# Performance work log

Measured on AMD Instinct MI355X. Metric: run time of the kernel, lower is better.

The kernel has to match this reference:

```python
import jax, jax.numpy as jnp
import numpy as np

B, TE, TD, EH, DH = 128, 512, 128, 512, 512
K_CNN, C_CNN = 7, 105

def setup_inputs() -> dict:
    key = jax.random.key(0)
    ks = jax.random.split(key, 20)
    n = lambda k, shp: jax.random.normal(k, shp, dtype=jnp.float32) * 0.05
    return {
        "LSTM": jax.random.normal(ks[0], (B, TE, EH), dtype=jnp.float32),
        "CNNs": jax.random.normal(ks[1], (B, K_CNN, C_CNN), dtype=jnp.float32),
        "Wa_w": n(ks[2], (TD, DH)), "Wa_b": n(ks[3], (TD,)),
        "Ua_w": n(ks[4], (TE, EH)), "Ua_b": n(ks[5], (TE,)),
        "va_w": n(ks[6], (1, TE + TD)), "va_b": n(ks[7], (1,)),
        "phi_w": n(ks[8], (EH, TE)), "phi_b": n(ks[9], (EH,)),
        "Wih": n(ks[10], (4 * DH, C_CNN + EH)), "Whh": n(ks[11], (4 * DH, DH)),
        "bih": n(ks[12], (4 * DH,)), "bhh": n(ks[13], (4 * DH,)),
        "wij_w": n(ks[14], (K_CNN, DH + C_CNN)), "wij_b": n(ks[15], (K_CNN,)),
        "s_i": jax.random.uniform(ks[16], (B, DH), dtype=jnp.float32),
        "m_i": jax.random.uniform(ks[17], (B, DH), dtype=jnp.float32),
    }

def reference(LSTM, CNNs, Wa_w, Wa_b, Ua_w, Ua_b, va_w, va_b, phi_w, phi_b,
              Wih, Whh, bih, bhh, wij_w, wij_b, s_i, m_i):
    Bn, Te, Eh = LSTM.shape
    Td = Wa_w.shape[0]
    Dh = s_i.shape[1]
    # delta_i_j for all j: strict lower-triangular one-hots [Te, Te]
    Dm = jnp.tril(jnp.ones((Te, Te), LSTM.dtype), k=-1)
    phi = Dm @ phi_w.T + phi_b                     # [Te, Eh]
    ph = phi[None, :, :] * LSTM                    # [B, Te, Eh] phi_delta * LSTM[:, j]
    Ua = jnp.einsum('bte,se->bts', ph, Ua_w) + Ua_b  # [B, Te, Te]
    Wa = s_i @ Wa_w.T + Wa_b                       # [B, Td] (same for all i, j)
    cat = jnp.concatenate([jnp.broadcast_to(Wa[:, None, :], (Bn, Te, Td)), Ua], axis=-1)
    Cw = jnp.tanh(cat) * va_w[0]                   # [B, Te, Td+Te]
    # one-hot mask picks index i + Te - j; v_a reduces to a single gathered term + bias
    idx = jnp.arange(Td)[:, None] + Te - jnp.arange(Te)[None, :]   # [Td, Te]
    e = Cw[:, jnp.arange(Te)[None, :], idx] + va_b[0]              # [B, Td, Te]
    a = jax.nn.softmax(e, axis=-1)
    c_i = jnp.einsum('bit,bte->bie', a, LSTM)      # [B, Td, Eh]
    # CNN attention (same for all decoder steps; note non-standard normalizer kept faithfully)
    w_cnn, w_s = wij_w[:, :C_CNN], wij_w[:, C_CNN:]
    ep = jnp.tanh(jnp.einsum('bkc,kc->bk', CNNs, w_cnn) + s_i @ w_s.T + wij_b)  # [B, K]
    ap = jnp.exp(ep) / jnp.sum(ep)
    c_p = jnp.einsum('bk,bkc->bc', ap, CNNs)       # [B, C_CNN]
    # LSTMCell with fixed (s_i, m_i) state => all decoder steps vectorize over i
    x = jnp.concatenate([c_i, jnp.broadcast_to(c_p[:, None, :], (Bn, Td, C_CNN))], axis=-1)
    gates = jnp.einsum('bid,gd->big', x, Wih) + bih + (s_i @ Whh.T + bhh)[:, None, :]
    ig, fg, gg, og = jnp.split(gates, 4, axis=-1)
    cnew = jax.nn.sigmoid(fg) * m_i[:, None, :] + jax.nn.sigmoid(ig) * jnp.tanh(gg)
    h = jax.nn.sigmoid(og) * jnp.tanh(cnew)        # [B, Td, Dh]
    return h
```

## Files before the change

### kernel.cpp

```cpp
#include <hip/hip_runtime.h>
#include <hip/hip_bf16.h>

#define B_   128
#define TE_  512
#define TD_  128
#define EH_  512
#define DH_  512
#define KC_  7
#define CC_  105
#define G_   2048
#define KX_  617
#define KP_  640

typedef __attribute__((ext_vector_type(8))) short bf16x8;
typedef __attribute__((ext_vector_type(4))) float f32x4;

__device__ __forceinline__ float sigm(float x){ return 1.f/(1.f + __expf(-x)); }
__device__ __forceinline__ float tanhf_fast(float x){
  float e = __expf(2.f*x);
  return 1.f - 2.f/(e + 1.f);
}

__device__ __forceinline__ unsigned short f2bf(float f){
  unsigned int u = __float_as_uint(f);
  unsigned int r = (u + 0x7fffu + ((u >> 16) & 1u)) >> 16;
  return (unsigned short)r;
}

__device__ __forceinline__ float dot512f(const float* a, const float* b) {
  const float4* a4 = (const float4*)a; const float4* b4 = (const float4*)b;
  float acc = 0.f;
  #pragma unroll 8
  for (int q = 0; q < 128; ++q) {
    float4 x = a4[q], y = b4[q];
    acc += x.x*y.x + x.y*y.y + x.z*y.z + x.w*y.w;
  }
  return acc;
}

static const size_t OFF_PHI  = 0;
static const size_t OFF_WA   = OFF_PHI  + (size_t)TE_*EH_*4;
static const size_t OFF_HPRE = OFF_WA   + (size_t)B_*TD_*4;
static const size_t OFF_EP   = OFF_HPRE + (size_t)B_*G_*4;
static const size_t OFF_CP   = OFF_EP   + 4096;
static const size_t OFF_ET   = ((OFF_CP + (size_t)B_*CC_*4 + 255)/256)*256;
static const size_t OFF_STAT = OFF_ET + (size_t)B_*TE_*TD_*4;
static const size_t OFF_P    = ((OFF_STAT + (size_t)2*B_*TD_*4 + 255)/256)*256;
static const size_t OFF_LT   = OFF_P  + (size_t)B_*TD_*TE_*2;
static const size_t OFF_WR   = OFF_LT + (size_t)B_*TE_*EH_*2;
static const size_t OFF_PT   = OFF_P;
static const size_t OFF_SUM  = OFF_PT + (size_t)TE_*EH_*4;

__global__ __launch_bounds__(256) void k_trw(const float* __restrict__ phi_w,
                                             float* __restrict__ phiT) {
  int e0 = blockIdx.x * 64, t0 = blockIdx.y * 64;
  __shared__ float tile[64][65];
  int tid = threadIdx.x;
  int r = tid >> 2, c16 = (tid & 3) * 16;
  const float4* src = (const float4*)(phi_w + (size_t)(e0 + r)*TE_ + t0 + c16);
  float4 v0 = src[0], v1 = src[1], v2 = src[2], v3 = src[3];
  *(float4*)&tile[r][c16]    = v0;
  *(float4*)&tile[r][c16+4]  = v1;
  *(float4*)&tile[r][c16+8]  = v2;
  *(float4*)&tile[r][c16+12] = v3;
  __syncthreads();
  float o[16];
  #pragma unroll
  for (int j = 0; j < 16; ++j) o[j] = tile[c16+j][r];
  float* dst = phiT + (size_t)(t0 + r)*EH_ + e0 + c16;
  *(float4*)dst      = *(float4*)&o[0];
  *(float4*)(dst+4)  = *(float4*)&o[4];
  *(float4*)(dst+8)  = *(float4*)&o[8];
  *(float4*)(dst+12) = *(float4*)&o[12];
}

__global__ void k_phiA(const float* __restrict__ phiT, float* __restrict__ phi,
                       float* __restrict__ sums) {
  int e = blockIdx.x * 256 + threadIdx.x;
  int z = blockIdx.y;
  float acc = 0.f;
  for (int t = z*64; t < z*64 + 64; ++t) {
    phi[(size_t)t*EH_ + e] = acc;
    acc += phiT[(size_t)t*EH_ + e];
  }
  sums[z*EH_ + e] = acc;
}
__global__ void k_phiB(const float* __restrict__ sums, const float* __restrict__ phi_b,
                       float* __restrict__ phi) {
  int e = blockIdx.x * 256 + threadIdx.x;
  int z = blockIdx.y;
  float off = phi_b[e];
  for (int zz = 0; zz < z; ++zz) off += sums[zz*EH_ + e];
  for (int t = z*64; t < z*64 + 64; ++t)
    phi[(size_t)t*EH_ + e] += off;
}

__global__ void k_wa(const float* __restrict__ s_i, const float* __restrict__ Wa_w,
                     const float* __restrict__ Wa_b, const float* __restrict__ va_w,
                     float* __restrict__ wa) {
  int id = blockIdx.x * blockDim.x + threadIdx.x;
  int b = id >> 7, d = id & 127;
  float acc = Wa_b[d] + dot512f(s_i + (size_t)b*DH_, Wa_w + (size_t)d*DH_);
  wa[id] = tanhf_fast(acc) * va_w[d];
}

__global__ void k_hpre(const float* __restrict__ s_i, const float* __restrict__ Whh,
                       const float* __restrict__ bih, const float* __restrict__ bhh,
                       float* __restrict__ hpre) {
  int id = blockIdx.x * blockDim.x + threadIdx.x;
  int b = id >> 11, g = id & 2047;
  hpre[id] = bih[g] + bhh[g] + dot512f(s_i + (size_t)b*DH_, Whh + (size_t)g*DH_);
}

__global__ __launch_bounds__(256) void k_ep(const float* __restrict__ CNNs,
                                            const float* __restrict__ wij_w,
                                            const float* __restrict__ wij_b,
                                            const float* __restrict__ s_i,
                                            float* __restrict__ ep) {
  int gw = blockIdx.x * 4 + (threadIdx.x >> 6);
  int lane = threadIdx.x & 63;
  if (gw >= B_*KC_) return;
  int b = gw / KC_, k = gw % KC_;
  const float* cr = CNNs + (size_t)(b*KC_ + k)*CC_;
  const float* wr = wij_w + (size_t)k*KX_;
  float acc = 0.f;
  for (int c = lane; c < CC_; c += 64) acc += cr[c] * wr[c];
  const float* sr = s_i + (size_t)b*DH_;
  const float* wsr = wr + CC_;
  #pragma unroll
  for (int j = 0; j < 8; ++j) { int h = lane + j*64; acc += sr[h] * wsr[h]; }
  #pragma unroll
  for (int m = 32; m; m >>= 1) acc += __shfl_xor(acc, m, 64);
  if (lane == 0) ep[gw] = tanhf_fast(acc + wij_b[k]);
}

__global__ void k_cnn_fin(const float* __restrict__ ep, const float* __restrict__ CNNs,
                          float* __restrict__ cp) {
  __shared__ float red[1024];
  __shared__ float apl[B_*KC_];
  int tid = threadIdx.x;
  red[tid] = (tid < B_*KC_) ? ep[tid] : 0.f;
  __syncthreads();
  for (int off = 512; off > 0; off >>= 1) {
    if (tid < off) red[tid] += red[tid + off];
    __syncthreads();
  }
  float S = red[0];
  if (tid < B_*KC_) apl[tid] = __expf(ep[tid]) / S;
  __syncthreads();
  for (int idx = tid; idx < B_*CC_; idx += blockDim.x) {
    int b = idx / CC_, c = idx % CC_;
    float acc = 0.f;
    #pragma unroll
    for (int k = 0; k < KC_; ++k)
      acc += apl[b*KC_ + k] * CNNs[(size_t)(b*KC_ + k)*CC_ + c];
    cp[idx] = acc;
  }
}

__global__ void k_cvtW(const float* __restrict__ Wih, unsigned short* __restrict__ Wr) {
  int id = blockIdx.x * 256 + threadIdx.x;
  int nr = id / 80, c8 = (id % 80) * 8;
  int gate = nr & 3, dh = nr >> 2;
  const float* src = Wih + (size_t)(gate*DH_ + dh)*KX_;
  unsigned short o[8];
  #pragma unroll
  for (int j = 0; j < 8; ++j) {
    int col = c8 + j;
    o[j] = (col < KX_) ? f2bf(src[col]) : 0;
  }
  *(uint4*)(Wr + (size_t)nr*KP_ + c8) = *(uint4*)o;
}

__global__ __launch_bounds__(256) void k_ltrans(const float* __restrict__ LSTM,
                                                unsigned short* __restrict__ LT) {
  int e0 = blockIdx.x * 64, t0 = blockIdx.y * 64, b = blockIdx.z;
  __shared__ float tile[64][65];
  int tid = threadIdx.x;
  int tt = tid >> 2, c16 = (tid & 3) * 16;
  const float4* src = (const float4*)(LSTM + ((size_t)b*TE_ + t0 + tt)*EH_ + e0 + c16);
  float4 v0 = src[0], v1 = src[1], v2 = src[2], v3 = src[3];
  *(float4*)&tile[tt][c16]    = v0;
  *(float4*)&tile[tt][c16+4]  = v1;
  *(float4*)&tile[tt][c16+8]  = v2;
  *(float4*)&tile[tt][c16+12] = v3;
  __syncthreads();
  int e = tid >> 2, t16 = (tid & 3) * 16;
  unsigned short o[16];
  #pragma unroll
  for (int j = 0; j < 16; ++j) o[j] = f2bf(tile[t16+j][e]);
  unsigned short* dst = LT + ((size_t)b*EH_ + e0 + e)*TE_ + t0 + t16;
  *(uint4*)dst     = *(uint4*)&o[0];
  *(uint4*)(dst+8) = *(uint4*)&o[8];
}

#define BMM_M 64
#define LDA_  40
#define LDB_  40
__global__ __launch_bounds__(256) void k_bandmm(const float* __restrict__ LSTM,
                                                const float* __restrict__ phi,
                                                const float* __restrict__ Ua_w,
                                                const float* __restrict__ Ua_b,
                                                const float* __restrict__ va_w,
                                                const float* __restrict__ va_b,
                                                const float* __restrict__ wa,
                                                float* __restrict__ ET) {
  int t0 = blockIdx.x * BMM_M;
  int b  = blockIdx.y;
  int s_base = 321 - t0;
  __shared__ short sA[BMM_M * LDA_];
  __shared__ short sB[192 * LDB_];
  int tid = threadIdx.x;
  int wave = tid >> 6, lane = tid & 63;
  int quad = lane >> 4, l16 = lane & 15;

  f32x4 acc[4][3];
  #pragma unroll
  for (int m = 0; m < 4; ++m)
    #pragma unroll
    for (int n = 0; n < 3; ++n)
      acc[m][n] = (f32x4){0.f, 0.f, 0.f, 0.f};

  int arow = tid >> 2;
  int ach  = (tid & 3) * 8;
  int aq   = ach >> 2;

  const float4* baseL = (const float4*)(LSTM + ((size_t)b*TE_ + t0 + arow)*EH_);
  const float4* baseP = (const float4*)(phi + (size_t)(t0 + arow)*EH_);
  const float4* baseU[3];
  int brow[3], bch[3];
  #pragma unroll
  for (int c = 0; c < 3; ++c) {
    int idx = c*256 + tid;
    brow[c] = idx >> 2;
    bch[c]  = (idx & 3) * 8;
    int s = s_base + brow[c];
    int sc = s < 0 ? 0 : (s > 511 ? 511 : s);
    baseU[c] = (const float4*)(Ua_w + (size_t)sc*EH_ + bch[c]);
  }

  float4 l0 = baseL[aq], l1 = baseL[aq+1], p0 = baseP[aq], p1 = baseP[aq+1];
  float4 u0[3], u1[3];
  #pragma unroll
  for (int c = 0; c < 3; ++c) { u0[c] = baseU[c][0]; u1[c] = baseU[c][1]; }

  for (int k0 = 0; k0 < EH_; k0 += 32) {
    unsigned short at[8];
    at[0]=f2bf(l0.x*p0.x); at[1]=f2bf(l0.y*p0.y); at[2]=f2bf(l0.z*p0.z); at[3]=f2bf(l0.w*p0.w);
    at[4]=f2bf(l1.x*p1.x); at[5]=f2bf(l1.y*p1.y); at[6]=f2bf(l1.z*p1.z); at[7]=f2bf(l1.w*p1.w);
    unsigned short bt[3][8];
    #pragma unroll
    for (int c = 0; c < 3; ++c) {
      bt[c][0]=f2bf(u0[c].x); bt[c][1]=f2bf(u0[c].y); bt[c][2]=f2bf(u0[c].z); bt[c][3]=f2bf(u0[c].w);
      bt[c][4]=f2bf(u1[c].x); bt[c][5]=f2bf(u1[c].y); bt[c][6]=f2bf(u1[c].z); bt[c][7]=f2bf(u1[c].w);
    }
    if (k0 + 32 < EH_) {
      int q = (k0 + 32) >> 2;
      l0 = baseL[q+aq]; l1 = baseL[q+aq+1]; p0 = baseP[q+aq]; p1 = baseP[q+aq+1];
      #pragma unroll
      for (int c = 0; c < 3; ++c) { u0[c] = baseU[c][q]; u1[c] = baseU[c][q+1]; }
    }
    __syncthreads();
    *(uint4*)&sA[arow*LDA_ + ach] = *(uint4*)at;
    #pragma unroll
    for (int c = 0; c < 3; ++c)
      *(uint4*)&sB[brow[c]*LDB_ + bch[c]] = *(uint4*)bt[c];
    __syncthreads();
    bf16x8 bfr[3];
    #pragma unroll
    for (int n = 0; n < 3; ++n)
      bfr[n] = *(const bf16x8*)&sB[(l16 + (wave*3 + n)*16)*LDB_ + quad*8];
    #pragma unroll
    for (int m = 0; m < 4; ++m) {
      bf16x8 af = *(const bf16x8*)&sA[(l16 + m*16)*LDA_ + quad*8];
      #pragma unroll
      for (int n = 0; n < 3; ++n)
        acc[m][n] = __builtin_amdgcn_mfma_f32_16x16x32_bf16(af, bfr[n], acc[m][n], 0, 0, 0);
    }
  }

  float vb = va_b[0];
  #pragma unroll
  for (int n = 0; n < 3; ++n) {
    int s = s_base + wave*48 + n*16 + l16;
    float ub = (s >= 0 && s < TE_) ? Ua_b[s] : 0.f;
    float vw = (s >= 0 && s < TE_) ? va_w[TD_ + s] : 0.f;
    #pragma unroll
    for (int m = 0; m < 4; ++m) {
      #pragma unroll
      for (int r = 0; r < 4; ++r) {
        int t = t0 + m*16 + quad*4 + r;
        int i = s + t - 384;
        if (i >= 0 && i < TD_) {
          float val;
          if (s >= 0) val = tanhf_fast(acc[m][n][r] + ub) * vw + vb;
          else        val = wa[b*TD_ + s + 128] + vb;
          ET[((size_t)b*TE_ + t)*TD_ + i] = val;
        }
      }
    }
  }
}

__global__ __launch_bounds__(256) void k_stats(const float* __restrict__ ET,
                                               float* __restrict__ stat) {
  int i0 = blockIdx.x * 64, b = blockIdx.y;
  __shared__ float red[4][64], smax[64];
  int tid = threadIdx.x;
  int q = tid >> 6, il = tid & 63;
  const float* col = ET + (size_t)b*TE_*TD_ + i0 + il;
  float m = -1e30f;
  for (int t = q*128; t < q*128 + 128; ++t) m = fmaxf(m, col[(size_t)t*TD_]);
  red[q][il] = m;
  __syncthreads();
  if (tid < 64) {
    float mm = fmaxf(fmaxf(red[0][tid], red[1][tid]), fmaxf(red[2][tid], red[3][tid]));
    smax[tid] = mm;
  }
  __syncthreads();
  float mm = smax[il];
  float s = 0.f;
  for (int t = q*128; t < q*128 + 128; ++t) s += __expf(col[(size_t)t*TD_] - mm);
  __syncthreads();
  red[q][il] = s;
  __syncthreads();
  if (tid < 64) {
    float ss = red[0][tid] + red[1][tid] + red[2][tid] + red[3][tid];
    stat[b*TD_ + i0 + tid] = smax[tid];
    stat[(size_t)B_*TD_ + b*TD_ + i0 + tid] = 1.f/ss;
  }
}

__global__ __launch_bounds__(256) void k_trP(const float* __restrict__ ET,
                                             const float* __restrict__ stat,
                                             unsigned short* __restrict__ P) {
  int t0 = blockIdx.x * 64, i0 = blockIdx.y * 64, b = blockIdx.z;
  __shared__ float tile[64][65];
  __shared__ float smL[64], svL[64];
  int tid = threadIdx.x;
  if (tid < 64) {
    smL[tid] = stat[b*TD_ + i0 + tid];
    svL[tid] = stat[(size_t)B_*TD_ + b*TD_ + i0 + tid];
  }
  int tt = tid >> 2, c16 = (tid & 3) * 16;
  const float4* src = (const float4*)(ET + ((size_t)b*TE_ + t0 + tt)*TD_ + i0 + c16);
  float4 v[4]; v[0] = src[0]; v[1] = src[1]; v[2] = src[2]; v[3] = src[3];
  __syncthreads();
  const float* vf = (const float*)v;
  #pragma unroll
  for (int j = 0; j < 16; ++j)
    tile[tt][c16+j] = __expf(vf[j] - smL[c16+j]) * svL[c16+j];
  __syncthreads();
  int i = tid >> 2, t16 = (tid & 3) * 16;
  unsigned short o[16];
  #pragma unroll
  for (int j = 0; j < 16; ++j) o[j] = f2bf(tile[t16+j][i]);
  unsigned short* dst = P + ((size_t)b*TD_ + i0 + i)*TE_ + t0 + t16;
  *(uint4*)dst     = *(uint4*)&o[0];
  *(uint4*)(dst+8) = *(uint4*)&o[8];
}

__global__ void k_cp_fill(const float* __restrict__ cp, unsigned short* __restrict__ X) {
  int id = blockIdx.x * 256 + threadIdx.x;
  int m = id >> 4, c8 = (id & 15) * 8;
  int b = m >> 7;
  unsigned short o[8];
  #pragma unroll
  for (int j = 0; j < 8; ++j) {
    int c = c8 + j;
    o[j] = (c < CC_) ? f2bf(cp[b*CC_ + c]) : 0;
  }
  *(uint4*)(X + (size_t)m*KP_ + EH_ + c8) = *(uint4*)o;
}

#define CI_LD 40
__global__ __launch_bounds__(256) void k_ci_mm(const unsigned short* __restrict__ P,
                                               const unsigned short* __restrict__ LT,
                                               unsigned short* __restrict__ X) {
  int b = blockIdx.x, e0 = blockIdx.y * 128;
  __shared__ short sA[128 * CI_LD];
  __shared__ short sB[128 * CI_LD];
  int tid = threadIdx.x;
  int wave = tid >> 6, lane = tid & 63, quad = lane >> 4, l16 = lane & 15;
  int wm = wave >> 1, wn = wave & 1;
  int row = tid >> 1, ho = (tid & 1) * 16;

  const unsigned short* pa = P + ((size_t)b*TD_ + row)*TE_ + ho;
  const unsigned short* pb = LT + ((size_t)b*EH_ + e0 + row)*TE_ + ho;

  f32x4 acc[4][4];
  #pragma unroll
  for (int m = 0; m < 4; ++m)
    #pragma unroll
    for (int n = 0; n < 4; ++n)
      acc[m][n] = (f32x4){0.f, 0.f, 0.f, 0.f};

  uint4 a0 = *(const uint4*)pa, a1 = *(const uint4*)(pa + 8);
  uint4 b0 = *(const uint4*)pb, b1 = *(const uint4*)(pb + 8);

  for (int k0 = 0; k0 < TE_; k0 += 32) {
    uint4 na0, na1, nb0, nb1;
    if (k0 + 32 < TE_) {
      na0 = *(const uint4*)(pa + k0 + 32); na1 = *(const uint4*)(pa + k0 + 40);
      nb0 = *(const uint4*)(pb + k0 + 32); nb1 = *(const uint4*)(pb + k0 + 40);
    }
    __syncthreads();
    *(uint4*)&sA[row*CI_LD + ho]     = a0;
    *(uint4*)&sA[row*CI_LD + ho + 8] = a1;
    *(uint4*)&sB[row*CI_LD + ho]     = b0;
    *(uint4*)&sB[row*CI_LD + ho + 8] = b1;
    __syncthreads();
    bf16x8 bfr[4];
    #pragma unroll
    for (int n = 0; n < 4; ++n)
      bfr[n] = *(const bf16x8*)&sB[(wn*64 + n*16 + l16)*CI_LD + quad*8];
    #pragma unroll
    for (int m = 0; m < 4; ++m) {
      bf16x8 af = *(const bf16x8*)&sA[(wm*64 + m*16 + l16)*CI_LD + quad*8];
      #pragma unroll
      for (int n = 0; n < 4; ++n)
        acc[m][n] = __builtin_amdgcn_mfma_f32_16x16x32_bf16(af, bfr[n], acc[m][n], 0, 0, 0);
    }
    a0 = na0; a1 = na1; b0 = nb0; b1 = nb1;
  }

  #pragma unroll
  for (int m = 0; m < 4; ++m) {
    int i = wm*64 + m*16 + quad*4;
    #pragma unroll
    for (int n = 0; n < 4; ++n) {
      int e = e0 + wn*64 + n*16 + l16;
      unsigned short* xp = X + ((size_t)b*TD_ + i)*KP_ + e;
      #pragma unroll
      for (int r = 0; r < 4; ++r)
        xp[(size_t)r*KP_] = f2bf(acc[m][n][r]);
    }
  }
}

__global__ __launch_bounds__(256) void k_gates_mm(const unsigned short* __restrict__ Wr,
                                                  const unsigned short* __restrict__ X,
                                                  const float* __restrict__ hpre,
                                                  const float* __restrict__ m_i,
                                                  float* __restrict__ out) {
  int g0 = blockIdx.x * 128;
  int mi0 = blockIdx.y * 128;
  __shared__ short sA[128 * CI_LD];
  __shared__ short sB[128 * CI_LD];
  int tid = threadIdx.x;
  int wave = tid >> 6, lane = tid & 63, quad = lane >> 4, l16 = lane & 15;
  int wg = wave >> 1, wmi = wave & 1;
  int row = tid >> 1, ho = (tid & 1) * 16;

  const unsigned short* pa = Wr + (size_t)(g0 + row)*KP_ + ho;
  const unsigned short* pb = X + (size_t)(mi0 + row)*KP_ + ho;

  f32x4 acc[4][4];
  #pragma unroll
  for (int m = 0; m < 4; ++m)
    #pragma unroll
    for (int n = 0; n < 4; ++n)
      acc[m][n] = (f32x4){0.f, 0.f, 0.f, 0.f};

  uint4 a0 = *(const uint4*)pa, a1 = *(const uint4*)(pa + 8);
  uint4 b0 = *(const uint4*)pb, b1 = *(const uint4*)(pb + 8);

  for (int k0 = 0; k0 < KP_; k0 += 32) {
    uint4 na0, na1, nb0, nb1;
    if (k0 + 32 < KP_) {
      na0 = *(const uint4*)(pa + k0 + 32); na1 = *(const uint4*)(pa + k0 + 40);
      nb0 = *(const uint4*)(pb + k0 + 32); nb1 = *(const uint4*)(pb + k0 + 40);
    }
    __syncthreads();
    *(uint4*)&sA[row*CI_LD + ho]     = a0;
    *(uint4*)&sA[row*CI_LD + ho + 8] = a1;
    *(uint4*)&sB[row*CI_LD + ho]     = b0;
    *(uint4*)&sB[row*CI_LD + ho + 8] = b1;
    __syncthreads();
    bf16x8 bfr[4];
    #pragma unroll
    for (int n = 0; n < 4; ++n)
      bfr[n] = *(const bf16x8*)&sB[(wmi*64 + n*16 + l16)*CI_LD + quad*8];
    #pragma unroll
    for (int m = 0; m < 4; ++m) {
      bf16x8 af = *(const bf16x8*)&sA[(wg*64 + m*16 + l16)*CI_LD + quad*8];
      #pragma unroll
      for (int n = 0; n < 4; ++n)
        acc[m][n] = __builtin_amdgcn_mfma_f32_16x16x32_bf16(af, bfr[n], acc[m][n], 0, 0, 0);
    }
    a0 = na0; a1 = na1; b0 = nb0; b1 = nb1;
  }

  int bbk = mi0 >> 7;
  const float* hp = hpre + (size_t)bbk*G_;
  #pragma unroll
  for (int m = 0; m < 4; ++m) {
    int dh = (g0 >> 2) + wg*16 + m*4 + quad;
    float h0 = hp[dh], h1 = hp[DH_ + dh], h2 = hp[2*DH_ + dh], h3 = hp[3*DH_ + dh];
    float miv = m_i[(size_t)bbk*DH_ + dh];
    #pragma unroll
    for (int n = 0; n < 4; ++n) {
      int mi = mi0 + wmi*64 + n*16 + l16;
      float ig = acc[m][n][0] + h0;
      float fg = acc[m][n][1] + h1;
      float gg = acc[m][n][2] + h2;
      float og = acc[m][n][3] + h3;
      float c  = sigm(fg)*miv + sigm(ig)*tanhf_fast(gg);
      float h  = sigm(og)*tanhf_fast(c);
      out[(size_t)mi*DH_ + dh] = h;
    }
  }
}

extern "C" void kernel_launch(void* const* d_in, const int* in_sizes, int n_in,
                              void* d_out, int out_size, void* d_ws, size_t ws_size,
                              hipStream_t stream) {
  (void)in_sizes; (void)n_in; (void)out_size; (void)ws_size;
  const float* LSTM  = (const float*)d_in[0];
  const float* CNNs  = (const float*)d_in[1];
  const float* Wa_w  = (const float*)d_in[2];
  const float* Wa_b  = (const float*)d_in[3];
  const float* Ua_w  = (const float*)d_in[4];
  const float* Ua_b  = (const float*)d_in[5];
  const float* va_w  = (const float*)d_in[6];
  const float* va_b  = (const float*)d_in[7];
  const float* phi_w = (const float*)d_in[8];
  const float* phi_b = (const float*)d_in[9];
  const float* Wih   = (const float*)d_in[10];
  const float* Whh   = (const float*)d_in[11];
  const float* bih   = (const float*)d_in[12];
  const float* bhh   = (const float*)d_in[13];
  const float* wij_w = (const float*)d_in[14];
  const float* wij_b = (const float*)d_in[15];
  const float* s_i   = (const float*)d_in[16];
  const float* m_i   = (const float*)d_in[17];
  float* out = (float*)d_out;
  char* ws = (char*)d_ws;

  float* phi  = (float*)(ws + OFF_PHI);
  float* wa   = (float*)(ws + OFF_WA);
  float* hpre = (float*)(ws + OFF_HPRE);
  float* ep   = (float*)(ws + OFF_EP);
  float* cp   = (float*)(ws + OFF_CP);
  float* stat = (float*)(ws + OFF_STAT);
  float* ET   = (float*)(ws + OFF_ET);
  unsigned short* X  = (unsigned short*)(ws + OFF_ET);
  unsigned short* P  = (unsigned short*)(ws + OFF_P);
  unsigned short* LT = (unsigned short*)(ws + OFF_LT);
  unsigned short* Wr = (unsigned short*)(ws + OFF_WR);
  float* phiT        = (float*)(ws + OFF_PT);
  float* sums        = (float*)(ws + OFF_SUM);

  k_trw     <<<dim3(8,8),      dim3(256),  0, stream>>>(phi_w, phiT);
  k_phiA    <<<dim3(2,8),      dim3(256),  0, stream>>>(phiT, phi, sums);
  k_phiB    <<<dim3(2,8),      dim3(256),  0, stream>>>(sums, phi_b, phi);
  k_wa      <<<dim3(64),       dim3(256),  0, stream>>>(s_i, Wa_w, Wa_b, va_w, wa);
  k_hpre    <<<dim3(1024),     dim3(256),  0, stream>>>(s_i, Whh, bih, bhh, hpre);
  k_ep      <<<dim3(224),      dim3(256),  0, stream>>>(CNNs, wij_w, wij_b, s_i, ep);
  k_cnn_fin <<<dim3(1),        dim3(1024), 0, stream>>>(ep, CNNs, cp);
  k_cvtW    <<<dim3(640),      dim3(256),  0, stream>>>(Wih, Wr);
  k_ltrans  <<<dim3(8,8,128),  dim3(256),  0, stream>>>(LSTM, LT);
  k_bandmm  <<<dim3(8,128),    dim3(256),  0, stream>>>(LSTM, phi, Ua_w, Ua_b, va_w, va_b, wa, ET);
  k_stats   <<<dim3(2,128),    dim3(256),  0, stream>>>(ET, stat);
  k_trP     <<<dim3(8,2,128),  dim3(256),  0, stream>>>(ET, stat, P);
  k_cp_fill <<<dim3(1024),     dim3(256),  0, stream>>>(cp, X);
  k_ci_mm   <<<dim3(128,4),    dim3(256),  0, stream>>>(P, LT, X);
  k_gates_mm<<<dim3(16,128),   dim3(256),  0, stream>>>(Wr, X, hpre, m_i, out);
}
```

Before: 575.9 us.

## Rewrite gates GEMM with 256x256 tiles, direct-to-LDS loads, pre-convert Ua to bf16

The gates GEMM is replaced with a 512-thread kernel using 256x256 output tiles, K-tiles of 64, double-buffered LDS filled via global_load_lds with an XOR swizzle, and setprio around the MFMA bursts. The larger tile is meant to improve data reuse, and the async LDS loads cut register staging. Separately, Ua_w is converted to bf16 once in a new small kernel, so the band matmul loads half the bytes and skips per-iteration conversion. The trade-offs are much higher LDS use per block (128KB), more registers, and fewer blocks (512) to spread across the CUs.

```diff
diff --git a/kernel.cpp b/kernel.cpp
--- a/kernel.cpp
+++ b/kernel.cpp
@@ -11,6 +11,7 @@
 #define G_   2048
 #define KX_  617
 #define KP_  640
+#define GNT  10
 
 typedef __attribute__((ext_vector_type(8))) short bf16x8;
 typedef __attribute__((ext_vector_type(4))) float f32x4;
@@ -36,6 +37,12 @@
     acc += x.x*y.x + x.y*y.y + x.z*y.z + x.w*y.w;
   }
   return acc;
+}
+
+typedef __attribute__((address_space(3))) unsigned int lds_u32_t;
+typedef __attribute__((address_space(1))) const unsigned int glb_u32_t;
+__device__ __forceinline__ void gload16(const void* g, void* l) {
+  __builtin_amdgcn_global_load_lds((glb_u32_t*)g, (lds_u32_t*)l, 16, 0, 0);
 }
 
 static const size_t OFF_PHI  = 0;
@@ -50,6 +57,7 @@
 static const size_t OFF_WR   = OFF_LT + (size_t)B_*TE_*EH_*2;
 static const size_t OFF_PT   = OFF_P;
 static const size_t OFF_SUM  = OFF_PT + (size_t)TE_*EH_*4;
+static const size_t OFF_UB   = OFF_P + (size_t)1536*1024;
 
 __global__ __launch_bounds__(256) void k_trw(const float* __restrict__ phi_w,
                                              float* __restrict__ phiT) {
@@ -172,6 +180,15 @@
   *(uint4*)(Wr + (size_t)nr*KP_ + c8) = *(uint4*)o;
 }
 
+__global__ void k_cvtU(const float* __restrict__ Ua_w, unsigned short* __restrict__ Ub) {
+  int id = blockIdx.x * 256 + threadIdx.x;
+  const float4* s = (const float4*)Ua_w + (size_t)id*2;
+  float4 a = s[0], b = s[1];
+  unsigned short o[8] = {f2bf(a.x),f2bf(a.y),f2bf(a.z),f2bf(a.w),
+                         f2bf(b.x),f2bf(b.y),f2bf(b.z),f2bf(b.w)};
+  *(uint4*)(Ub + (size_t)id*8) = *(uint4*)o;
+}
+
 __global__ __launch_bounds__(256) void k_ltrans(const float* __restrict__ LSTM,
                                                 unsigned short* __restrict__ LT) {
   int e0 = blockIdx.x * 64, t0 = blockIdx.y * 64, b = blockIdx.z;
@@ -199,7 +216,7 @@
 #define LDB_  40
 __global__ __launch_bounds__(256) void k_bandmm(const float* __restrict__ LSTM,
                                                 const float* __restrict__ phi,
-                                                const float* __restrict__ Ua_w,
+                                                const unsigned short* __restrict__ Ub,
                                                 const float* __restrict__ Ua_b,
                                                 const float* __restrict__ va_w,
                                                 const float* __restrict__ va_b,
@@ -227,7 +244,7 @@
 
   const float4* baseL = (const float4*)(LSTM + ((size_t)b*TE_ + t0 + arow)*EH_);
   const float4* baseP = (const float4*)(phi + (size_t)(t0 + arow)*EH_);
-  const float4* baseU[3];
+  const unsigned short* ubase[3];
   int brow[3], bch[3];
   #pragma unroll
   for (int c = 0; c < 3; ++c) {
@@ -236,35 +253,32 @@
     bch[c]  = (idx & 3) * 8;
     int s = s_base + brow[c];
     int sc = s < 0 ? 0 : (s > 511 ? 511 : s);
-    baseU[c] = (const float4*)(Ua_w + (size_t)sc*EH_ + bch[c]);
+    ubase[c] = Ub + (size_t)sc*EH_ + bch[c];
   }
 
   float4 l0 = baseL[aq], l1 = baseL[aq+1], p0 = baseP[aq], p1 = baseP[aq+1];
-  float4 u0[3], u1[3];
-  #pragma unroll
-  for (int c = 0; c < 3; ++c) { u0[c] = baseU[c][0]; u1[c] = baseU[c][1]; }
+  uint4 ub0[3];
+  #pragma unroll
+  for (int c = 0; c < 3; ++c) ub0[c] = *(const uint4*)(ubase[c]);
 
   for (int k0 = 0; k0 < EH_; k0 += 32) {
     unsigned short at[8];
     at[0]=f2bf(l0.x*p0.x); at[1]=f2bf(l0.y*p0.y); at[2]=f2bf(l0.z*p0.z); at[3]=f2bf(l0.w*p0.w);
     at[4]=f2bf(l1.x*p1.x); at[5]=f2bf(l1.y*p1.y); at[6]=f2bf(l1.z*p1.z); at[7]=f2bf(l1.w*p1.w);
-    unsigned short bt[3][8];
-    #pragma unroll
-    for (int c = 0; c < 3; ++c) {
-      bt[c][0]=f2bf(u0[c].x); bt[c][1]=f2bf(u0[c].y); bt[c][2]=f2bf(u0[c].z); bt[c][3]=f2bf(u0[c].w);
-      bt[c][4]=f2bf(u1[c].x); bt[c][5]=f2bf(u1[c].y); bt[c][6]=f2bf(u1[c].z); bt[c][7]=f2bf(u1[c].w);
-    }
+    uint4 ust[3];
+    #pragma unroll
+    for (int c = 0; c < 3; ++c) ust[c] = ub0[c];
     if (k0 + 32 < EH_) {
       int q = (k0 + 32) >> 2;
       l0 = baseL[q+aq]; l1 = baseL[q+aq+1]; p0 = baseP[q+aq]; p1 = baseP[q+aq+1];
       #pragma unroll
-      for (int c = 0; c < 3; ++c) { u0[c] = baseU[c][q]; u1[c] = baseU[c][q+1]; }
+      for (int c = 0; c < 3; ++c) ub0[c] = *(const uint4*)(ubase[c] + k0 + 32);
     }
     __syncthreads();
     *(uint4*)&sA[arow*LDA_ + ach] = *(uint4*)at;
     #pragma unroll
     for (int c = 0; c < 3; ++c)
-      *(uint4*)&sB[brow[c]*LDB_ + bch[c]] = *(uint4*)bt[c];
+      *(uint4*)&sB[brow[c]*LDB_ + bch[c]] = ust[c];
     __syncthreads();
     bf16x8 bfr[3];
     #pragma unroll
@@ -438,73 +452,94 @@
   }
 }
 
-__global__ __launch_bounds__(256) void k_gates_mm(const unsigned short* __restrict__ Wr,
-                                                  const unsigned short* __restrict__ X,
-                                                  const float* __restrict__ hpre,
-                                                  const float* __restrict__ m_i,
-                                                  float* __restrict__ out) {
-  int g0 = blockIdx.x * 128;
-  int mi0 = blockIdx.y * 128;
-  __shared__ short sA[128 * CI_LD];
-  __shared__ short sB[128 * CI_LD];
-  int tid = threadIdx.x;
-  int wave = tid >> 6, lane = tid & 63, quad = lane >> 4, l16 = lane & 15;
-  int wg = wave >> 1, wmi = wave & 1;
-  int row = tid >> 1, ho = (tid & 1) * 16;
-
-  const unsigned short* pa = Wr + (size_t)(g0 + row)*KP_ + ho;
-  const unsigned short* pb = X + (size_t)(mi0 + row)*KP_ + ho;
-
-  f32x4 acc[4][4];
-  #pragma unroll
-  for (int m = 0; m < 4; ++m)
-    #pragma unroll
-    for (int n = 0; n < 4; ++n)
-      acc[m][n] = (f32x4){0.f, 0.f, 0.f, 0.f};
-
-  uint4 a0 = *(const uint4*)pa, a1 = *(const uint4*)(pa + 8);
-  uint4 b0 = *(const uint4*)pb, b1 = *(const uint4*)(pb + 8);
-
-  for (int k0 = 0; k0 < KP_; k0 += 32) {
-    uint4 na0, na1, nb0, nb1;
-    if (k0 + 32 < KP_) {
-      na0 = *(const uint4*)(pa + k0 + 32); na1 = *(const uint4*)(pa + k0 + 40);
-      nb0 = *(const uint4*)(pb + k0 + 32); nb1 = *(const uint4*)(pb + k0 + 40);
-    }
-    __syncthreads();
-    *(uint4*)&sA[row*CI_LD + ho]     = a0;
-    *(uint4*)&sA[row*CI_LD + ho + 8] = a1;
-    *(uint4*)&sB[row*CI_LD + ho]     = b0;
-    *(uint4*)&sB[row*CI_LD + ho + 8] = b1;
-    __syncthreads();
-    bf16x8 bfr[4];
-    #pragma unroll
-    for (int n = 0; n < 4; ++n)
-      bfr[n] = *(const bf16x8*)&sB[(wmi*64 + n*16 + l16)*CI_LD + quad*8];
-    #pragma unroll
-    for (int m = 0; m < 4; ++m) {
-      bf16x8 af = *(const bf16x8*)&sA[(wg*64 + m*16 + l16)*CI_LD + quad*8];
+__global__ __launch_bounds__(512, 2) void k_gates8(const unsigned short* __restrict__ Wr,
+                                                   const unsigned short* __restrict__ X,
+                                                   const float* __restrict__ hpre,
+                                                   const float* __restrict__ m_i,
+                                                   float* __restrict__ out) {
+  __shared__ short lds[4 * 256 * 64];
+  const int g0  = blockIdx.x * 256;
+  const int mi0 = blockIdx.y * 256;
+  const int tid  = threadIdx.x;
+  const int wave = tid >> 6, lane = tid & 63;
+  const int l16 = lane & 15, quad = lane >> 4;
+  const int wr = wave >> 2, wc = wave & 3;
+
+  const int srow8 = lane >> 3;
+  const int sch   = (lane & 7) ^ srow8;
+  const unsigned short* gA = Wr + (size_t)(g0  + wave*8 + srow8) * KP_ + sch*8;
+  const unsigned short* gB = X  + (size_t)(mi0 + wave*8 + srow8) * KP_ + sch*8;
+  short* lA0 = lds;
+  short* lB0 = lds + 16384;
+  short* lA1 = lds + 32768;
+  short* lB1 = lds + 49152;
+
+  f32x4 acc[8][4];
+  #pragma unroll
+  for (int m = 0; m < 8; ++m)
+    #pragma unroll
+    for (int n = 0; n < 4; ++n) acc[m][n] = (f32x4){0.f, 0.f, 0.f, 0.f};
+
+  auto stage = [&](int kt, int bf) {
+    short* la = bf ? lA1 : lA0;
+    short* lb = bf ? lB1 : lB0;
+    const unsigned short* ga = gA + kt*64;
+    const unsigned short* gb = gB + kt*64;
+    #pragma unroll
+    for (int r = 0; r < 4; ++r) {
+      gload16(ga + (size_t)r*64*KP_, la + (r*8 + wave)*512);
+      gload16(gb + (size_t)r*64*KP_, lb + (r*8 + wave)*512);
+    }
+  };
+
+  stage(0, 0);
+  __syncthreads();
+
+  const int x7 = l16 & 7;
+  for (int kt = 0; kt < GNT; ++kt) {
+    const int cur = kt & 1;
+    if (kt + 1 < GNT) stage(kt + 1, cur ^ 1);
+    const short* la = cur ? lA1 : lA0;
+    const short* lb = cur ? lB1 : lB0;
+    #pragma unroll
+    for (int ks = 0; ks < 2; ++ks) {
+      const int ck = ((((ks << 2) | quad) ^ x7) << 3);
+      bf16x8 bv[4];
       #pragma unroll
       for (int n = 0; n < 4; ++n)
-        acc[m][n] = __builtin_amdgcn_mfma_f32_16x16x32_bf16(af, bfr[n], acc[m][n], 0, 0, 0);
-    }
-    a0 = na0; a1 = na1; b0 = nb0; b1 = nb1;
-  }
-
-  int bbk = mi0 >> 7;
-  const float* hp = hpre + (size_t)bbk*G_;
-  #pragma unroll
-  for (int m = 0; m < 4; ++m) {
-    int dh = (g0 >> 2) + wg*16 + m*4 + quad;
+        bv[n] = *(const bf16x8*)&lb[(wc*64 + n*16 + l16)*64 + ck];
+      #pragma unroll
+      for (int qm = 0; qm < 2; ++qm) {
+        bf16x8 av[4];
+        #pragma unroll
+        for (int m = 0; m < 4; ++m)
+          av[m] = *(const bf16x8*)&la[(wr*128 + qm*64 + m*16 + l16)*64 + ck];
+        __builtin_amdgcn_s_setprio(1);
+        #pragma unroll
+        for (int m = 0; m < 4; ++m)
+          #pragma unroll
+          for (int n = 0; n < 4; ++n)
+            acc[qm*4 + m][n] = __builtin_amdgcn_mfma_f32_16x16x32_bf16(av[m], bv[n], acc[qm*4 + m][n], 0, 0, 0);
+        __builtin_amdgcn_s_setprio(0);
+      }
+    }
+    __syncthreads();
+  }
+
+  const int bb = (mi0 >> 7) + (wc >> 1);
+  const float* hp = hpre + (size_t)bb * G_;
+  #pragma unroll
+  for (int M = 0; M < 8; ++M) {
+    const int dh = (g0 >> 2) + wr*32 + M*4 + quad;
     float h0 = hp[dh], h1 = hp[DH_ + dh], h2 = hp[2*DH_ + dh], h3 = hp[3*DH_ + dh];
-    float miv = m_i[(size_t)bbk*DH_ + dh];
+    float miv = m_i[(size_t)bb*DH_ + dh];
     #pragma unroll
     for (int n = 0; n < 4; ++n) {
-      int mi = mi0 + wmi*64 + n*16 + l16;
-      float ig = acc[m][n][0] + h0;
-      float fg = acc[m][n][1] + h1;
-      float gg = acc[m][n][2] + h2;
-      float og = acc[m][n][3] + h3;
+      int mi = mi0 + wc*64 + n*16 + l16;
+      float ig = acc[M][n][0] + h0;
+      float fg = acc[M][n][1] + h1;
+      float gg = acc[M][n][2] + h2;
+      float og = acc[M][n][3] + h3;
       float c  = sigm(fg)*miv + sigm(ig)*tanhf_fast(gg);
       float h  = sigm(og)*tanhf_fast(c);
       out[(size_t)mi*DH_ + dh] = h;
@@ -550,6 +585,7 @@
   unsigned short* Wr = (unsigned short*)(ws + OFF_WR);
   float* phiT        = (float*)(ws + OFF_PT);
   float* sums        = (float*)(ws + OFF_SUM);
+  unsigned short* Ub = (unsigned short*)(ws + OFF_UB);
 
   k_trw     <<<dim3(8,8),      dim3(256),  0, stream>>>(phi_w, phiT);
   k_phiA    <<<dim3(2,8),      dim3(256),  0, stream>>>(phiT, phi, sums);
@@ -559,11 +595,12 @@
   k_ep      <<<dim3(224),      dim3(256),  0, stream>>>(CNNs, wij_w, wij_b, s_i, ep);
   k_cnn_fin <<<dim3(1),        dim3(1024), 0, stream>>>(ep, CNNs, cp);
   k_cvtW    <<<dim3(640),      dim3(256),  0, stream>>>(Wih, Wr);
+  k_cvtU    <<<dim3(128),      dim3(256),  0, stream>>>(Ua_w, Ub);
   k_ltrans  <<<dim3(8,8,128),  dim3(256),  0, stream>>>(LSTM, LT);
-  k_bandmm  <<<dim3(8,128),    dim3(256),  0, stream>>>(LSTM, phi, Ua_w, Ua_b, va_w, va_b, wa, ET);
+  k_bandmm  <<<dim3(8,128),    dim3(256),  0, stream>>>(LSTM, phi, Ub, Ua_b, va_w, va_b, wa, ET);
   k_stats   <<<dim3(2,128),    dim3(256),  0, stream>>>(ET, stat);
   k_trP     <<<dim3(8,2,128),  dim3(256),  0, stream>>>(ET, stat, P);
   k_cp_fill <<<dim3(1024),     dim3(256),  0, stream>>>(cp, X);
   k_ci_mm   <<<dim3(128,4),    dim3(256),  0, stream>>>(P, LT, X);
-  k_gates_mm<<<dim3(16,128),   dim3(256),  0, stream>>>(Wr, X, hpre, m_i, out);
-}
+  k_gates8  <<<dim3(8,64),     dim3(512),  0, stream>>>(Wr, X, hpre, m_i, out);
+}
```

New measurement: 650.6 us. 13.0% more time.
